# Optimization experiments

Hardware: AMD Instinct MI355X
Metric: run time of the kernel (lower is better)

Reference implementation:

```python
import jax, jax.numpy as jnp
import numpy as np

B, S, H = 2, 2048, 2048
NH, NKV, HD = 32, 8, 64
N_REP = NH // NKV
ROPE_THETA = 10000.0
NEG_INF = -1e9


def rotate_half(x):
    h = x.shape[-1] // 2
    return jnp.concatenate([-x[..., h:], x[..., :h]], axis=-1)


def rope_cos_sin(seq_len, head_dim, base, dtype):
    inv_freq = 1.0 / (base ** (jnp.arange(0, head_dim, 2, dtype=jnp.float32) / head_dim))
    t = jnp.arange(seq_len, dtype=jnp.float32)
    freqs = jnp.einsum('s,d->sd', t, inv_freq)          # [S, HD/2]
    emb = jnp.concatenate([freqs, freqs], axis=-1)       # [S, HD]
    return jnp.cos(emb).astype(dtype), jnp.sin(emb).astype(dtype)


def setup_inputs() -> dict:
    key = jax.random.key(0)
    ks = jax.random.split(key, 5)
    sc = 0.02
    return {
        'hidden_states': jax.random.normal(ks[0], (B, S, H), dtype=jnp.float32),
        'Wq': jax.random.normal(ks[1], (NH * HD, H), dtype=jnp.float32) * sc,
        'Wk': jax.random.normal(ks[2], (NKV * HD, H), dtype=jnp.float32) * sc,
        'Wv': jax.random.normal(ks[3], (NKV * HD, H), dtype=jnp.float32) * sc,
        'Wo': jax.random.normal(ks[4], (H, NH * HD), dtype=jnp.float32) * sc,
    }


def reference(hidden_states, Wq, Wk, Wv, Wo):
    bsz, q_len, _ = hidden_states.shape
    dtype = hidden_states.dtype

    # QKV projections (torch Linear: x @ W^T), reshape to [B, heads, S, HD]
    q = jnp.einsum('bsh,oh->bso', hidden_states, Wq).reshape(bsz, q_len, NH, HD).transpose(0, 2, 1, 3)
    k = jnp.einsum('bsh,oh->bso', hidden_states, Wk).reshape(bsz, q_len, NKV, HD).transpose(0, 2, 1, 3)
    v = jnp.einsum('bsh,oh->bso', hidden_states, Wv).reshape(bsz, q_len, NKV, HD).transpose(0, 2, 1, 3)

    # RoPE (position_ids = arange)
    cos, sin = rope_cos_sin(q_len, HD, ROPE_THETA, dtype)
    cos = cos[None, None]  # [1,1,S,HD]
    sin = sin[None, None]
    q = q * cos + rotate_half(q) * sin
    k = k * cos + rotate_half(k) * sin

    # GQA repeat_kv (repeat_interleave over head dim)
    k = jnp.repeat(k, N_REP, axis=1)  # [B, NH, S, HD]
    v = jnp.repeat(v, N_REP, axis=1)

    # scaled dot-product attention with causal mask
    scores = jnp.einsum('bhqd,bhkd->bhqk', q, k) / jnp.sqrt(jnp.asarray(HD, dtype))
    causal = jnp.tril(jnp.ones((q_len, q_len), dtype=bool))
    scores = jnp.where(causal[None, None], scores, jnp.asarray(NEG_INF, dtype))
    attn = jax.nn.softmax(scores.astype(jnp.float32), axis=-1).astype(dtype)

    out = jnp.einsum('bhqk,bhkd->bhqd', attn, v)
    out = out.transpose(0, 2, 1, 3).reshape(bsz, q_len, NH * HD)
    return jnp.einsum('bso,ho->bsh', out, Wo)
```

## Files before the change

kernel.cpp:

```cpp
#include <hip/hip_runtime.h>
#include <hip/hip_bf16.h>
#include <cstdint>
#include <cmath>

#define B_   2
#define S_   2048
#define H_   2048
#define NH_  32
#define NKV_ 8
#define HD_  64
#define CSTR 3072

using bf16x8 = __attribute__((ext_vector_type(8))) short;
using f32x4  = __attribute__((ext_vector_type(4))) float;

#define MFMA16(a, b, c) __builtin_amdgcn_mfma_f32_16x16x32_bf16((a), (b), (c), 0, 0, 0)

__device__ __forceinline__ short f2bf(float f) {
  uint32_t u = __float_as_uint(f);
  uint32_t r = (u + 0x7fffu + ((u >> 16) & 1u)) >> 16;
  return (short)r;
}
__device__ __forceinline__ float bf2f(short s) {
  return __uint_as_float(((uint32_t)(uint16_t)s) << 16);
}
__device__ __forceinline__ uint32_t f2bf_pk(float a, float b) {
#if __has_builtin(__builtin_amdgcn_cvt_pk_bf16_f32)
  auto r = __builtin_amdgcn_cvt_pk_bf16_f32(a, b);
  uint32_t u; __builtin_memcpy(&u, &r, sizeof(u));
  return u;
#else
  uint32_t ua = (__float_as_uint(a) + 0x8000u) >> 16;
  uint32_t ub = (__float_as_uint(b) + 0x8000u) >> 16;
  return ua | (ub << 16);
#endif
}
__device__ __forceinline__ float fast_exp2(float x) {
#if __has_builtin(__builtin_amdgcn_exp2f)
  return __builtin_amdgcn_exp2f(x);
#else
  return exp2f(x);
#endif
}

__device__ __forceinline__ void gload_lds16(const void* g, void* l) {
  __builtin_amdgcn_global_load_lds((const __attribute__((address_space(1))) void*)g,
                                   (__attribute__((address_space(3))) void*)l, 16, 0, 0);
}

struct Cvt5Args {
  const float *s0, *s1, *s2, *s3, *s4;
  short *d0, *d1, *d2, *d3, *d4;
};
#define CV0 2097152
#define CV1 (CV0 + 1048576)
#define CV2 (CV1 + 262144)
#define CV3 (CV2 + 262144)
#define CV4 (CV3 + 1048576)
__global__ void cvt5_kernel(Cvt5Args a) {
  int i = blockIdx.x * blockDim.x + threadIdx.x;
  const float* s; short* d; int off;
  if      (i < CV0) { s = a.s0; d = a.d0; off = i; }
  else if (i < CV1) { s = a.s1; d = a.d1; off = i - CV0; }
  else if (i < CV2) { s = a.s2; d = a.d2; off = i - CV1; }
  else if (i < CV3) { s = a.s3; d = a.d3; off = i - CV2; }
  else              { s = a.s4; d = a.d4; off = i - CV3; }
  const float4 v = ((const float4*)s)[off];
  uint2 o;
  o.x = (uint32_t)(uint16_t)f2bf(v.x) | ((uint32_t)(uint16_t)f2bf(v.y) << 16);
  o.y = (uint32_t)(uint16_t)f2bf(v.z) | ((uint32_t)(uint16_t)f2bf(v.w) << 16);
  ((uint2*)d)[off] = o;
}

__global__ __launch_bounds__(512, 4) void gemm_qkvcat(
    const short* __restrict__ A, const short* __restrict__ Bcat,
    short* __restrict__ Ccat)
{
  __shared__ __align__(16) short As[2][128 * 64];
  __shared__ __align__(16) short Bs[2][192 * 64];

  const long tileM = (long)blockIdx.y * 128;
  const long tileN = (long)blockIdx.x * 192;
  const int  K = 2048;

  const int tid  = threadIdx.x;
  const int lane = tid & 63;
  const int quad = lane >> 4;
  const int l15  = lane & 15;
  const int wave = tid >> 6;
  const int wm   = (wave >> 2) * 64;
  const int wn   = (wave & 3) * 48;
  const int xsw  = l15 & 7;

  f32x4 acc[4][3];
#pragma unroll
  for (int i = 0; i < 4; ++i)
#pragma unroll
    for (int j = 0; j < 3; ++j) acc[i][j] = f32x4{0.f, 0.f, 0.f, 0.f};

  const int cS = (tid & 7) ^ ((tid >> 3) & 7);
  const short* gA[2]; const short* gB[3];
#pragma unroll
  for (int p = 0; p < 2; ++p)
    gA[p] = A + (tileM + (tid >> 3) + 64 * p) * K + cS * 8;
#pragma unroll
  for (int p = 0; p < 3; ++p)
    gB[p] = Bcat + (tileN + (tid >> 3) + 64 * p) * K + cS * 8;

  auto stage = [&](int buf, int t) {
    const long ko = (long)t * 64;
    short* la = &As[buf][0];
    short* lb = &Bs[buf][0];
#pragma unroll
    for (int p = 0; p < 2; ++p)
      gload_lds16(gA[p] + ko, la + (tid + p * 512) * 8);
#pragma unroll
    for (int p = 0; p < 3; ++p)
      gload_lds16(gB[p] + ko, lb + (tid + p * 512) * 8);
  };

  const int NT = K / 64;
  stage(0, 0);
  asm volatile("s_waitcnt vmcnt(0)" ::: "memory");
  asm volatile("s_barrier" ::: "memory");

  bf16x8 af[2][2], bfr[3][2];

  auto ldA = [&](const short* Ab, int half) {
#pragma unroll
    for (int m = 0; m < 2; ++m) {
      const int r = wm + (half * 2 + m) * 16 + l15;
#pragma unroll
      for (int kk = 0; kk < 2; ++kk)
        af[m][kk] = *(const bf16x8*)&Ab[r * 64 + (((kk * 4 + quad) ^ xsw) << 3)];
    }
  };
  auto ldB = [&](const short* Bb) {
#pragma unroll
    for (int n = 0; n < 3; ++n) {
      const int r = wn + n * 16 + l15;
#pragma unroll
      for (int kk = 0; kk < 2; ++kk)
        bfr[n][kk] = *(const bf16x8*)&Bb[r * 64 + (((kk * 4 + quad) ^ xsw) << 3)];
    }
  };
  auto mma = [&](int half) {
    __builtin_amdgcn_s_setprio(1);
#pragma unroll
    for (int m = 0; m < 2; ++m)
#pragma unroll
      for (int n = 0; n < 3; ++n)
#pragma unroll
        for (int kk = 0; kk < 2; ++kk)
          acc[half * 2 + m][n] = MFMA16(af[m][kk], bfr[n][kk], acc[half * 2 + m][n]);
    __builtin_amdgcn_s_setprio(0);
  };

  for (int t = 0; t < NT; ++t) {
    const int cur = t & 1;
    const short* Ab = &As[cur][0];
    const short* Bb = &Bs[cur][0];

    if (t + 1 < NT) stage(cur ^ 1, t + 1);
    ldB(Bb); ldA(Ab, 0); mma(0);
    asm volatile("s_barrier" ::: "memory");
    ldA(Ab, 1); mma(1);
    asm volatile("s_waitcnt vmcnt(0)" ::: "memory");
    asm volatile("s_waitcnt lgkmcnt(0)" ::: "memory");
    asm volatile("s_barrier" ::: "memory");
  }

#pragma unroll
  for (int i = 0; i < 4; ++i)
#pragma unroll
    for (int j = 0; j < 3; ++j)
#pragma unroll
      for (int r = 0; r < 4; ++r) {
        long row = tileM + wm + i * 16 + quad * 4 + r;
        long col = tileN + wn + j * 16 + l15;
        Ccat[row * CSTR + col] = f2bf(acc[i][j][r]);
      }
}

__global__ __launch_bounds__(512, 4) void gemm_out(
    const short* __restrict__ A, const short* __restrict__ Bm,
    float* __restrict__ Cf)
{
  __shared__ __align__(16) short As[2][128 * 64];
  __shared__ __align__(16) short Bs[2][128 * 64];

  const int N = 2048, K = 2048;
  const long tileM = (long)blockIdx.y * 128;
  const long tileN = (long)blockIdx.x * 128;

  const int tid  = threadIdx.x;
  const int lane = tid & 63;
  const int quad = lane >> 4;
  const int l15  = lane & 15;
  const int wave = tid >> 6;
  const int wm   = (wave >> 2) * 64;
  const int wn   = (wave & 3) * 32;
  const int xsw  = l15 & 7;

  f32x4 acc[4][2];
#pragma unroll
  for (int i = 0; i < 4; ++i)
#pragma unroll
    for (int j = 0; j < 2; ++j) acc[i][j] = f32x4{0.f, 0.f, 0.f, 0.f};

  const int cS = (tid & 7) ^ ((tid >> 3) & 7);
  const short* gA[2]; const short* gB[2];
#pragma unroll
  for (int p = 0; p < 2; ++p) {
    gA[p] = A  + (tileM + (tid >> 3) + 64 * p) * K + cS * 8;
    gB[p] = Bm + (tileN + (tid >> 3) + 64 * p) * K + cS * 8;
  }

  auto stage = [&](int buf, int t) {
    const long ko = (long)t * 64;
    short* la = &As[buf][0];
    short* lb = &Bs[buf][0];
#pragma unroll
    for (int p = 0; p < 2; ++p) {
      gload_lds16(gA[p] + ko, la + (tid + p * 512) * 8);
      gload_lds16(gB[p] + ko, lb + (tid + p * 512) * 8);
    }
  };

  const int NT = K / 64;
  stage(0, 0);
  asm volatile("s_waitcnt vmcnt(0)" ::: "memory");
  asm volatile("s_barrier" ::: "memory");

  bf16x8 af[2][2], bfr[2][2];

  auto ldA = [&](const short* Ab, int half) {
#pragma unroll
    for (int m = 0; m < 2; ++m) {
      const int r = wm + (half * 2 + m) * 16 + l15;
#pragma unroll
      for (int kk = 0; kk < 2; ++kk)
        af[m][kk] = *(const bf16x8*)&Ab[r * 64 + (((kk * 4 + quad) ^ xsw) << 3)];
    }
  };
  auto ldB = [&](const short* Bb) {
#pragma unroll
    for (int n = 0; n < 2; ++n) {
      const int r = wn + n * 16 + l15;
#pragma unroll
      for (int kk = 0; kk < 2; ++kk)
        bfr[n][kk] = *(const bf16x8*)&Bb[r * 64 + (((kk * 4 + quad) ^ xsw) << 3)];
    }
  };
  auto mma = [&](int half) {
    __builtin_amdgcn_s_setprio(1);
#pragma unroll
    for (int m = 0; m < 2; ++m)
#pragma unroll
      for (int n = 0; n < 2; ++n)
#pragma unroll
        for (int kk = 0; kk < 2; ++kk)
          acc[half * 2 + m][n] = MFMA16(af[m][kk], bfr[n][kk], acc[half * 2 + m][n]);
    __builtin_amdgcn_s_setprio(0);
  };

  for (int t = 0; t < NT; ++t) {
    const int cur = t & 1;
    const short* Ab = &As[cur][0];
    const short* Bb = &Bs[cur][0];

    if (t + 1 < NT) stage(cur ^ 1, t + 1);
    ldB(Bb); ldA(Ab, 0); mma(0);
    asm volatile("s_barrier" ::: "memory");
    ldA(Ab, 1); mma(1);
    asm volatile("s_waitcnt vmcnt(0)" ::: "memory");
    asm volatile("s_waitcnt lgkmcnt(0)" ::: "memory");
    asm volatile("s_barrier" ::: "memory");
  }

#pragma unroll
  for (int i = 0; i < 4; ++i)
#pragma unroll
    for (int j = 0; j < 2; ++j)
#pragma unroll
      for (int r = 0; r < 4; ++r) {
        long row = tileM + wm + i * 16 + quad * 4 + r;
        long col = tileN + wn + j * 16 + l15;
        Cf[row * N + col] = acc[i][j][r];
      }
}

#define ROPE_BLOCKS 2560
__global__ void rope_vtrans_kernel(short* __restrict__ Ccat, short* __restrict__ Vt) {
  __shared__ short tile[64][65];
  if (blockIdx.x < ROPE_BLOCKS) {
    const int QT = (B_ * S_) * NH_ * 4;
    int t = blockIdx.x * blockDim.x + threadIdx.x;
    long base; int g; float scale; int row;
    if (t < QT) {
      row = t >> 7; int rem = t & 127, head = rem >> 2; g = rem & 3;
      base = (long)row * CSTR + head * HD_;
      scale = 0.125f * 1.44269504f;
    } else {
      int t2 = t - QT;
      row = t2 >> 5; int rem = t2 & 31, head = rem >> 2; g = rem & 3;
      base = (long)row * CSTR + 2048 + head * HD_;
      scale = 1.0f;
    }
    const int s = row & (S_ - 1);
    const int i0 = g * 8;
    union V8 { bf16x8 v; short e[8]; };
    V8 x0, x1, y0, y1;
    x0.v = *(const bf16x8*)&Ccat[base + i0];
    x1.v = *(const bf16x8*)&Ccat[base + i0 + 32];
#pragma unroll
    for (int j = 0; j < 8; ++j) {
      const int i = i0 + j;
      float invr = exp2f((float)i * -0.41524101f) * 0.15915494309f;
      float rev = (float)s * invr;
      rev -= floorf(rev);
      float ar = rev * 6.28318530718f;
      float c = __cosf(ar), sn = __sinf(ar);
      float a = bf2f(x0.e[j]);
      float b = bf2f(x1.e[j]);
      y0.e[j] = f2bf((a * c - b * sn) * scale);
      y1.e[j] = f2bf((b * c + a * sn) * scale);
    }
    *(bf16x8*)&Ccat[base + i0]      = y0.v;
    *(bf16x8*)&Ccat[base + i0 + 32] = y1.v;
  } else {
    int blk = blockIdx.x - ROPE_BLOCKS;
    int s0 = (blk & 31) * 64;
    int h  = (blk >> 5) & 7;
    int b  = blk >> 8;
    int tid = threadIdx.x;
#pragma unroll
    for (int it = 0; it < 16; ++it) {
      int idx = tid + it * 256;
      int r = idx >> 6, c = idx & 63;
      tile[r][c] = Ccat[((long)(b * S_ + s0 + r)) * CSTR + 2560 + h * HD_ + c];
    }
    __syncthreads();
#pragma unroll
    for (int it = 0; it < 16; ++it) {
      int idx = tid + it * 256;
      int d = idx >> 6, s = idx & 63;
      int slot = (s & 0x20) | (((s >> 2) & 3) << 3) | (((s >> 4) & 1) << 2) | (s & 3);
      Vt[((long)((b * NKV_ + h) * HD_ + d)) * S_ + s0 + slot] = tile[s][d];
    }
  }
}

__global__ __launch_bounds__(256, 3) void attn_kernel(
    const short* __restrict__ Ccat, const short* __restrict__ Vt,
    short* __restrict__ O)
{
  const int l    = (int)blockIdx.x + 8 * (int)blockIdx.y;
  const int r8   = l & 7;
  const int m    = l >> 3;
  const int kvcol = r8 + 8 * (m >> 5);
  const int idx  = m & 31;
  const int b    = kvcol >> 3;
  const int hkv  = kvcol & 7;
  const int h    = hkv * 4 + (idx >> 3);
  const int pair = idx & 7;

  const int tid = threadIdx.x, lane = tid & 63, w = tid >> 6;
  const int quad = lane >> 4, l15 = lane & 15;

  __shared__ __align__(16) short Ks[2][64 * 64];
  __shared__ __align__(16) short Vs[2][64 * 64];

  const short* kg = Ccat + ((long)(b * S_)) * CSTR + 2048 + hkv * HD_;
  const short* vg = Vt + ((long)((b * NKV_ + hkv) * HD_)) * S_;

  const int rK = tid >> 3;
  const int cC = (tid & 7) ^ (rK & 7);
  const short* kSrc = kg + (long)rK * CSTR + cC * 8;
  const short* vSrc = vg + (long)rK * S_ + cC * 8;
  short* kDst = &Ks[0][tid * 8];
  short* vDst = &Vs[0][tid * 8];

  auto stage = [&](int buf, int kb) {
    const long ko = (long)kb * 64 * CSTR;
    const long vo = (long)kb * 64;
    const int bo = buf * 4096;
    gload_lds16(kSrc + ko,              kDst + bo);
    gload_lds16(kSrc + ko + 32L * CSTR, kDst + bo + 2048);
    gload_lds16(vSrc + vo,              vDst + bo);
    gload_lds16(vSrc + vo + 32L * S_,   vDst + bo + 2048);
  };

  const int thr = w * 16 + l15;
  union U8 { uint32_t u[4]; bf16x8 v; };

  auto run_tile = [&](int qt) {
    const int kmax = 2 * qt + 1;
    const int qbase = qt * 128 + w * 16;
    const short* qb0 = Ccat + ((long)(b * S_ + qbase + l15)) * CSTR + h * HD_;
    const short* qb1 = qb0 + 64L * CSTR;
    const bf16x8 aq00 = *(const bf16x8*)(qb0 + quad * 8);
    const bf16x8 aq01 = *(const bf16x8*)(qb0 + 32 + quad * 8);
    const bf16x8 aq10 = *(const bf16x8*)(qb1 + quad * 8);
    const bf16x8 aq11 = *(const bf16x8*)(qb1 + 32 + quad * 8);

    f32x4 o0[4], o1[4];
#pragma unroll
    for (int i = 0; i < 4; ++i) {
      o0[i] = f32x4{0.f, 0.f, 0.f, 0.f};
      o1[i] = f32x4{0.f, 0.f, 0.f, 0.f};
    }
    f32x4 li0 = f32x4{0.f, 0.f, 0.f, 0.f};
    f32x4 li1 = f32x4{0.f, 0.f, 0.f, 0.f};

    stage(0, 0);
    asm volatile("s_waitcnt vmcnt(0)" ::: "memory");
    asm volatile("s_barrier" ::: "memory");

    int cur = 0;
    for (int kb = 0; kb <= kmax; ++kb) {
      if (kb < kmax) stage(cur ^ 1, kb + 1);
      const short* Kb = &Ks[cur][0];
      const short* Vb = &Vs[cur][0];
      const bool doF0 = (kb != kmax);

      f32x4 s0[4], s1[4];
      __builtin_amdgcn_s_setprio(1);
#pragma unroll
      for (int nt = 0; nt < 4; ++nt) {
        const int r = nt * 16 + l15;
        bf16x8 k0 = *(const bf16x8*)&Kb[(r * 8 + ((quad)     ^ (r & 7))) * 8];
        bf16x8 k1 = *(const bf16x8*)&Kb[(r * 8 + ((quad + 4) ^ (r & 7))) * 8];
        f32x4 t = f32x4{0.f, 0.f, 0.f, 0.f};
        t = MFMA16(k0, aq10, t);
        t = MFMA16(k1, aq11, t);
        s1[nt] = t;
        if (doF0) {
          f32x4 u = f32x4{0.f, 0.f, 0.f, 0.f};
          u = MFMA16(k0, aq00, u);
          u = MFMA16(k1, aq01, u);
          s0[nt] = u;
        }
      }
      __builtin_amdgcn_s_setprio(0);

      if (kb == kmax) {
#pragma unroll
        for (int nt = 0; nt < 4; ++nt) {
          const int base = nt * 16 + quad * 4;
#pragma unroll
          for (int rr = 0; rr < 4; ++rr)
            if (base + rr > thr) s1[nt][rr] = -1e30f;
        }
      }
      if (doF0 && kb == kmax - 1) {
#pragma unroll
        for (int nt = 0; nt < 4; ++nt) {
          const int base = nt * 16 + quad * 4;
#pragma unroll
          for (int rr = 0; rr < 4; ++rr)
            if (base + rr > thr) s0[nt][rr] = -1e30f;
        }
      }

      U8 p0[2], p1[2];
#pragma unroll
      for (int kt = 0; kt < 2; ++kt) {
        float e0 = fast_exp2(s1[2 * kt][0]),     e1 = fast_exp2(s1[2 * kt][1]);
        float e2 = fast_exp2(s1[2 * kt][2]),     e3 = fast_exp2(s1[2 * kt][3]);
        float e4 = fast_exp2(s1[2 * kt + 1][0]), e5 = fast_exp2(s1[2 * kt + 1][1]);
        float e6 = fast_exp2(s1[2 * kt + 1][2]), e7 = fast_exp2(s1[2 * kt + 1][3]);
        p1[kt].u[0] = f2bf_pk(e0, e1);
        p1[kt].u[1] = f2bf_pk(e2, e3);
        p1[kt].u[2] = f2bf_pk(e4, e5);
        p1[kt].u[3] = f2bf_pk(e6, e7);
        li1 += f32x4{e0, e1, e2, e3};
        li1 += f32x4{e4, e5, e6, e7};
      }
      if (doF0) {
#pragma unroll
        for (int kt = 0; kt < 2; ++kt) {
          float e0 = fast_exp2(s0[2 * kt][0]),     e1 = fast_exp2(s0[2 * kt][1]);
          float e2 = fast_exp2(s0[2 * kt][2]),     e3 = fast_exp2(s0[2 * kt][3]);
          float e4 = fast_exp2(s0[2 * kt + 1][0]), e5 = fast_exp2(s0[2 * kt + 1][1]);
          float e6 = fast_exp2(s0[2 * kt + 1][2]), e7 = fast_exp2(s0[2 * kt + 1][3]);
          p0[kt].u[0] = f2bf_pk(e0, e1);
          p0[kt].u[1] = f2bf_pk(e2, e3);
          p0[kt].u[2] = f2bf_pk(e4, e5);
          p0[kt].u[3] = f2bf_pk(e6, e7);
          li0 += f32x4{e0, e1, e2, e3};
          li0 += f32x4{e4, e5, e6, e7};
        }
      }

      __builtin_amdgcn_s_setprio(1);
#pragma unroll
      for (int kt = 0; kt < 2; ++kt) {
        bf16x8 vf[4];
#pragma unroll
        for (int dt = 0; dt < 4; ++dt)
          vf[dt] = *(const bf16x8*)&Vb[(dt * 16 + l15) * 64 +
                                       (((kt * 4 + quad) ^ (l15 & 7)) << 3)];
#pragma unroll
        for (int dt = 0; dt < 4; ++dt)
          o1[dt] = MFMA16(vf[dt], p1[kt].v, o1[dt]);
        if (doF0) {
#pragma unroll
          for (int dt = 0; dt < 4; ++dt)
            o0[dt] = MFMA16(vf[dt], p0[kt].v, o0[dt]);
        }
      }
      __builtin_amdgcn_s_setprio(0);

      asm volatile("s_waitcnt vmcnt(0)" ::: "memory");
      asm volatile("s_waitcnt lgkmcnt(0)" ::: "memory");
      asm volatile("s_barrier" ::: "memory");
      cur ^= 1;
    }

    auto epi = [&](f32x4 (&o)[4], const f32x4& li4, int qrow0) {
      float l2 = (li4[0] + li4[1]) + (li4[2] + li4[3]);
      l2 += __shfl_xor(l2, 16, 64);
      l2 += __shfl_xor(l2, 32, 64);
      float invl = 1.0f / l2;
      long orow = (long)(b * S_ + qrow0 + l15);
#pragma unroll
      for (int dt = 0; dt < 4; ++dt) {
        uint2 st;
        st.x = f2bf_pk(o[dt][0] * invl, o[dt][1] * invl);
        st.y = f2bf_pk(o[dt][2] * invl, o[dt][3] * invl);
        *(uint2*)&O[orow * (NH_ * HD_) + h * HD_ + dt * 16 + quad * 4] = st;
      }
    };
    epi(o1, li1, qbase + 64);
    epi(o0, li0, qbase);
  };

  run_tile(15 - pair);
  run_tile(pair);
}

extern "C" void kernel_launch(void* const* d_in, const int* in_sizes, int n_in,
                              void* d_out, int out_size, void* d_ws, size_t ws_size,
                              hipStream_t stream) {
  const float* hs = (const float*)d_in[0];
  const float* Wq = (const float*)d_in[1];
  const float* Wk = (const float*)d_in[2];
  const float* Wv = (const float*)d_in[3];
  const float* Wo = (const float*)d_in[4];
  float* out = (float*)d_out;

  char* p = (char*)d_ws;
  auto carve = [&](size_t elems) { short* r = (short*)p; p += elems * 2; return r; };
  short* Xb   = carve(8388608);
  short* Wcat = carve(6291456);
  short* Wob  = carve(4194304);
  short* Ccat = carve(12582912);
  short* Vtt  = carve(2097152);
  short* Om   = carve(8388608);

  short* Wqb = Wcat;
  short* Wkb = Wcat + 4194304;
  short* Wvb = Wcat + 5242880;

  Cvt5Args ca{hs, Wq, Wk, Wv, Wo, Xb, Wqb, Wkb, Wvb, Wob};
  cvt5_kernel<<<CV4 / 256, 256, 0, stream>>>(ca);

  gemm_qkvcat<<<dim3(16, 32), 512, 0, stream>>>(Xb, Wcat, Ccat);

  rope_vtrans_kernel<<<ROPE_BLOCKS + 512, 256, 0, stream>>>(Ccat, Vtt);

  attn_kernel<<<dim3(8, 64, 1), 256, 0, stream>>>(Ccat, Vtt, Om);

  gemm_out<<<dim3(16, 32), 512, 0, stream>>>(Om, Wob, out);
}
```

Baseline: 259.5 us.

## Split attention query tile across eight waves instead of two sub-tiles per wave

```diff
diff --git a/kernel.cpp b/kernel.cpp
--- a/kernel.cpp
+++ b/kernel.cpp
@@ -351,7 +351,7 @@
   }
 }
 
-__global__ __launch_bounds__(256, 3) void attn_kernel(
+__global__ __launch_bounds__(512, 4) void attn_kernel(
     const short* __restrict__ Ccat, const short* __restrict__ Vt,
     short* __restrict__ O)
 {
@@ -385,33 +385,27 @@
     const long ko = (long)kb * 64 * CSTR;
     const long vo = (long)kb * 64;
     const int bo = buf * 4096;
-    gload_lds16(kSrc + ko,              kDst + bo);
-    gload_lds16(kSrc + ko + 32L * CSTR, kDst + bo + 2048);
-    gload_lds16(vSrc + vo,              vDst + bo);
-    gload_lds16(vSrc + vo + 32L * S_,   vDst + bo + 2048);
-  };
-
-  const int thr = w * 16 + l15;
+    gload_lds16(kSrc + ko, kDst + bo);
+    gload_lds16(vSrc + vo, vDst + bo);
+  };
+
+  const int thr   = w * 16 + l15;
+  const bool lower = (w < 4);
+  const int thrW  = lower ? thr : thr - 64;
   union U8 { uint32_t u[4]; bf16x8 v; };
 
   auto run_tile = [&](int qt) {
     const int kmax = 2 * qt + 1;
-    const int qbase = qt * 128 + w * 16;
-    const short* qb0 = Ccat + ((long)(b * S_ + qbase + l15)) * CSTR + h * HD_;
-    const short* qb1 = qb0 + 64L * CSTR;
-    const bf16x8 aq00 = *(const bf16x8*)(qb0 + quad * 8);
-    const bf16x8 aq01 = *(const bf16x8*)(qb0 + 32 + quad * 8);
-    const bf16x8 aq10 = *(const bf16x8*)(qb1 + quad * 8);
-    const bf16x8 aq11 = *(const bf16x8*)(qb1 + 32 + quad * 8);
-
-    f32x4 o0[4], o1[4];
-#pragma unroll
-    for (int i = 0; i < 4; ++i) {
-      o0[i] = f32x4{0.f, 0.f, 0.f, 0.f};
-      o1[i] = f32x4{0.f, 0.f, 0.f, 0.f};
-    }
-    f32x4 li0 = f32x4{0.f, 0.f, 0.f, 0.f};
-    f32x4 li1 = f32x4{0.f, 0.f, 0.f, 0.f};
+    const int qbase = qt * 128;
+    const int qrow0 = qbase + w * 16;
+    const short* qb = Ccat + ((long)(b * S_ + qrow0 + l15)) * CSTR + h * HD_;
+    const bf16x8 aq0 = *(const bf16x8*)(qb + quad * 8);
+    const bf16x8 aq1 = *(const bf16x8*)(qb + 32 + quad * 8);
+
+    f32x4 o[4];
+#pragma unroll
+    for (int i = 0; i < 4; ++i) o[i] = f32x4{0.f, 0.f, 0.f, 0.f};
+    f32x4 li4 = f32x4{0.f, 0.f, 0.f, 0.f};
 
     stage(0, 0);
     asm volatile("s_waitcnt vmcnt(0)" ::: "memory");
@@ -422,95 +416,63 @@
       if (kb < kmax) stage(cur ^ 1, kb + 1);
       const short* Kb = &Ks[cur][0];
       const short* Vb = &Vs[cur][0];
-      const bool doF0 = (kb != kmax);
-
-      f32x4 s0[4], s1[4];
-      __builtin_amdgcn_s_setprio(1);
-#pragma unroll
-      for (int nt = 0; nt < 4; ++nt) {
-        const int r = nt * 16 + l15;
-        bf16x8 k0 = *(const bf16x8*)&Kb[(r * 8 + ((quad)     ^ (r & 7))) * 8];
-        bf16x8 k1 = *(const bf16x8*)&Kb[(r * 8 + ((quad + 4) ^ (r & 7))) * 8];
-        f32x4 t = f32x4{0.f, 0.f, 0.f, 0.f};
-        t = MFMA16(k0, aq10, t);
-        t = MFMA16(k1, aq11, t);
-        s1[nt] = t;
-        if (doF0) {
-          f32x4 u = f32x4{0.f, 0.f, 0.f, 0.f};
-          u = MFMA16(k0, aq00, u);
-          u = MFMA16(k1, aq01, u);
-          s0[nt] = u;
+      const bool doW = !(kb == kmax && lower);
+      const bool doMask = lower ? (kb == kmax - 1) : (kb == kmax);
+
+      if (doW) {
+        f32x4 s[4];
+        __builtin_amdgcn_s_setprio(1);
+#pragma unroll
+        for (int nt = 0; nt < 4; ++nt) {
+          const int r = nt * 16 + l15;
+          bf16x8 k0 = *(const bf16x8*)&Kb[(r * 8 + ((quad)     ^ (r & 7))) * 8];
+          bf16x8 k1 = *(const bf16x8*)&Kb[(r * 8 + ((quad + 4) ^ (r & 7))) * 8];
+          f32x4 t = f32x4{0.f, 0.f, 0.f, 0.f};
+          t = MFMA16(k0, aq0, t);
+          t = MFMA16(k1, aq1, t);
+          s[nt] = t;
         }
+        __builtin_amdgcn_s_setprio(0);
+
+        if (doMask) {
+#pragma unroll
+          for (int nt = 0; nt < 4; ++nt) {
+            const int base = nt * 16 + quad * 4;
+#pragma unroll
+            for (int rr = 0; rr < 4; ++rr)
+              if (base + rr > thrW) s[nt][rr] = -1e30f;
+          }
+        }
+
+        U8 p[2];
+#pragma unroll
+        for (int kt = 0; kt < 2; ++kt) {
+          float e0 = fast_exp2(s[2 * kt][0]),     e1 = fast_exp2(s[2 * kt][1]);
+          float e2 = fast_exp2(s[2 * kt][2]),     e3 = fast_exp2(s[2 * kt][3]);
+          float e4 = fast_exp2(s[2 * kt + 1][0]), e5 = fast_exp2(s[2 * kt + 1][1]);
+          float e6 = fast_exp2(s[2 * kt + 1][2]), e7 = fast_exp2(s[2 * kt + 1][3]);
+          p[kt].u[0] = f2bf_pk(e0, e1);
+          p[kt].u[1] = f2bf_pk(e2, e3);
+          p[kt].u[2] = f2bf_pk(e4, e5);
+          p[kt].u[3] = f2bf_pk(e6, e7);
+          li4 += f32x4{e0, e1, e2, e3};
+          li4 += f32x4{e4, e5, e6, e7};
+        }
+
+        __builtin_amdgcn_s_setprio(1);
+#pragma unroll
+        for (int kt = 0; kt < 2; ++kt) {
+          bf16x8 vf[4];
+#pragma unroll
+          for (int dt = 0; dt < 4; ++dt)
+            vf[dt] = *(const bf16x8*)&Vb[(dt * 16 + l15) * 64 +
+                                         (((kt * 4 + quad) ^ (l15 & 7)) << 3)];
+#pragma unroll
+          for (int dt = 0; dt < 4; ++dt)
+            o[dt] = MFMA16(vf[dt], p[kt].v, o[dt]);
+        }
+        __builtin_amdgcn_s_setprio(0);
       }
-      __builtin_amdgcn_s_setprio(0);
-
-      if (kb == kmax) {
-#pragma unroll
-        for (int nt = 0; nt < 4; ++nt) {
-          const int base = nt * 16 + quad * 4;
-#pragma unroll
-          for (int rr = 0; rr < 4; ++rr)
-            if (base + rr > thr) s1[nt][rr] = -1e30f;
-        }
-      }
-      if (doF0 && kb == kmax - 1) {
-#pragma unroll
-        for (int nt = 0; nt < 4; ++nt) {
-          const int base = nt * 16 + quad * 4;
-#pragma unroll
-          for (int rr = 0; rr < 4; ++rr)
-            if (base + rr > thr) s0[nt][rr] = -1e30f;
-        }
-      }
-
-      U8 p0[2], p1[2];
-#pragma unroll
-      for (int kt = 0; kt < 2; ++kt) {
-        float e0 = fast_exp2(s1[2 * kt][0]),     e1 = fast_exp2(s1[2 * kt][1]);
-        float e2 = fast_exp2(s1[2 * kt][2]),     e3 = fast_exp2(s1[2 * kt][3]);
-        float e4 = fast_exp2(s1[2 * kt + 1][0]), e5 = fast_exp2(s1[2 * kt + 1][1]);
-        float e6 = fast_exp2(s1[2 * kt + 1][2]), e7 = fast_exp2(s1[2 * kt + 1][3]);
-        p1[kt].u[0] = f2bf_pk(e0, e1);
-        p1[kt].u[1] = f2bf_pk(e2, e3);
-        p1[kt].u[2] = f2bf_pk(e4, e5);
-        p1[kt].u[3] = f2bf_pk(e6, e7);
-        li1 += f32x4{e0, e1, e2, e3};
-        li1 += f32x4{e4, e5, e6, e7};
-      }
-      if (doF0) {
-#pragma unroll
-        for (int kt = 0; kt < 2; ++kt) {
-          float e0 = fast_exp2(s0[2 * kt][0]),     e1 = fast_exp2(s0[2 * kt][1]);
-          float e2 = fast_exp2(s0[2 * kt][2]),     e3 = fast_exp2(s0[2 * kt][3]);
-          float e4 = fast_exp2(s0[2 * kt + 1][0]), e5 = fast_exp2(s0[2 * kt + 1][1]);
-          float e6 = fast_exp2(s0[2 * kt + 1][2]), e7 = fast_exp2(s0[2 * kt + 1][3]);
-          p0[kt].u[0] = f2bf_pk(e0, e1);
-          p0[kt].u[1] = f2bf_pk(e2, e3);
-          p0[kt].u[2] = f2bf_pk(e4, e5);
-          p0[kt].u[3] = f2bf_pk(e6, e7);
-          li0 += f32x4{e0, e1, e2, e3};
-          li0 += f32x4{e4, e5, e6, e7};
-        }
-      }
-
-      __builtin_amdgcn_s_setprio(1);
-#pragma unroll
-      for (int kt = 0; kt < 2; ++kt) {
-        bf16x8 vf[4];
-#pragma unroll
-        for (int dt = 0; dt < 4; ++dt)
-          vf[dt] = *(const bf16x8*)&Vb[(dt * 16 + l15) * 64 +
-                                       (((kt * 4 + quad) ^ (l15 & 7)) << 3)];
-#pragma unroll
-        for (int dt = 0; dt < 4; ++dt)
-          o1[dt] = MFMA16(vf[dt], p1[kt].v, o1[dt]);
-        if (doF0) {
-#pragma unroll
-          for (int dt = 0; dt < 4; ++dt)
-            o0[dt] = MFMA16(vf[dt], p0[kt].v, o0[dt]);
-        }
-      }
-      __builtin_amdgcn_s_setprio(0);
 
       asm volatile("s_waitcnt vmcnt(0)" ::: "memory");
       asm volatile("s_waitcnt lgkmcnt(0)" ::: "memory");
@@ -518,22 +480,18 @@
       cur ^= 1;
     }
 
-    auto epi = [&](f32x4 (&o)[4], const f32x4& li4, int qrow0) {
-      float l2 = (li4[0] + li4[1]) + (li4[2] + li4[3]);
-      l2 += __shfl_xor(l2, 16, 64);
-      l2 += __shfl_xor(l2, 32, 64);
-      float invl = 1.0f / l2;
-      long orow = (long)(b * S_ + qrow0 + l15);
-#pragma unroll
-      for (int dt = 0; dt < 4; ++dt) {
-        uint2 st;
-        st.x = f2bf_pk(o[dt][0] * invl, o[dt][1] * invl);
-        st.y = f2bf_pk(o[dt][2] * invl, o[dt][3] * invl);
-        *(uint2*)&O[orow * (NH_ * HD_) + h * HD_ + dt * 16 + quad * 4] = st;
-      }
-    };
-    epi(o1, li1, qbase + 64);
-    epi(o0, li0, qbase);
+    float l2 = (li4[0] + li4[1]) + (li4[2] + li4[3]);
+    l2 += __shfl_xor(l2, 16, 64);
+    l2 += __shfl_xor(l2, 32, 64);
+    float invl = 1.0f / l2;
+    long orow = (long)(b * S_ + qrow0 + l15);
+#pragma unroll
+    for (int dt = 0; dt < 4; ++dt) {
+      uint2 st;
+      st.x = f2bf_pk(o[dt][0] * invl, o[dt][1] * invl);
+      st.y = f2bf_pk(o[dt][2] * invl, o[dt][3] * invl);
+      *(uint2*)&O[orow * (NH_ * HD_) + h * HD_ + dt * 16 + quad * 4] = st;
+    }
   };
 
   run_tile(15 - pair);
@@ -570,7 +528,7 @@
 
   rope_vtrans_kernel<<<ROPE_BLOCKS + 512, 256, 0, stream>>>(Ccat, Vtt);
 
-  attn_kernel<<<dim3(8, 64, 1), 256, 0, stream>>>(Ccat, Vtt, Om);
+  attn_kernel<<<dim3(8, 64, 1), 512, 0, stream>>>(Ccat, Vtt, Om);
 
   gemm_out<<<dim3(16, 32), 512, 0, stream>>>(Om, Wob, out);
 }
```

New measurement: 261.3 us. No clear change (+0.7%).
